# Optimization experiments

Hardware: AMD Instinct MI355X
Metric: run time of the kernel (lower is better)

The kernel has to match this reference:

```python
import jax, jax.numpy as jnp
import numpy as np

N_CLASSES = 1000  # init kwarg n_classes
BIG = 1e24        # diagonal fill used by get_center_distances


def setup_inputs() -> dict:
    key = jax.random.key(0)
    k1, k2 = jax.random.split(key)
    embeddings = jax.random.normal(k1, (400000, 64), dtype=jnp.float32)
    target = jax.random.randint(k2, (400000,), 0, N_CLASSES)
    return {"embeddings": embeddings, "target": target}


def reference(embeddings, target):
    # Training-mode IILoss forward (returned loss does not depend on running buffers).
    n = embeddings.shape[0]
    ones = jnp.ones((n,), embeddings.dtype)
    counts = jax.ops.segment_sum(ones, target, num_segments=N_CLASSES)          # [C]
    sums = jax.ops.segment_sum(embeddings, target, num_segments=N_CLASSES)      # [C, D]
    mu = sums / jnp.maximum(counts, 1.0)[:, None]                                # per-class mean

    # intra_spread = sum_i ||e_i - mu[target_i]||^2 / n  (single fused pass)
    diff = embeddings - mu[target]
    intra_spread = jnp.sum(diff * diff) / n

    # pairwise squared distances between centers of classes present in the batch
    sq = jnp.sum(mu * mu, axis=1)                                                # [C]
    dists = sq[:, None] + sq[None, :] - 2.0 * (mu @ mu.T)                        # [C, C]
    present = counts > 0
    mask = present[:, None] & present[None, :] & ~jnp.eye(N_CLASSES, dtype=bool)
    dists = jnp.where(mask, dists, jnp.asarray(BIG, dists.dtype))
    inter_separation = -jnp.min(dists)
    return (intra_spread, inter_separation)
```

## Files before the change

kernel.cpp:

```cpp
#include <hip/hip_runtime.h>

#define NCLS 1000
#define DIM 64
#define CURW 32
#define SPLIT 4

struct Ws {
    int      counts[NCLS];
    unsigned minkey;
    unsigned pad_;
    int      offs[NCLS];
    float    mu[NCLS * DIM];
    float    sq[NCLS];
    int      cur[NCLS * CURW];
};

__device__ __forceinline__ unsigned fkey(float x) {
    unsigned b = __float_as_uint(x);
    return (b & 0x80000000u) ? ~b : (b | 0x80000000u);
}
__device__ __forceinline__ float funkey(unsigned k) {
    return (k & 0x80000000u) ? __uint_as_float(k & 0x7FFFFFFFu)
                             : __uint_as_float(~k);
}

__global__ __launch_bounds__(256) void k_hist(const int* __restrict__ tgt, int n, Ws* ws) {
    __shared__ int h[NCLS];
    for (int i = threadIdx.x; i < NCLS; i += 256) h[i] = 0;
    __syncthreads();
    const int n4 = n >> 2;
    const int4* t4 = reinterpret_cast<const int4*>(tgt);
    for (int i = blockIdx.x * 256 + threadIdx.x; i < n4; i += gridDim.x * 256) {
        const int4 v = t4[i];
        atomicAdd(&h[v.x], 1); atomicAdd(&h[v.y], 1);
        atomicAdd(&h[v.z], 1); atomicAdd(&h[v.w], 1);
    }
    if (blockIdx.x == 0)
        for (int r = (n4 << 2) + threadIdx.x; r < n; r += 256) atomicAdd(&h[tgt[r]], 1);
    __syncthreads();
    for (int i = threadIdx.x; i < NCLS; i += 256) {
        const int c = h[i];
        if (c) atomicAdd(&ws->counts[i], c);
    }
}

__global__ __launch_bounds__(1024) void k_scan(Ws* ws) {
    __shared__ int s[1024];
    const int t = threadIdx.x;
    const int myc = (t < NCLS) ? ws->counts[t] : 0;
    s[t] = myc;
    __syncthreads();
    for (int st = 1; st < 1024; st <<= 1) {
        const int v = (t >= st) ? s[t - st] : 0;
        __syncthreads();
        s[t] += v;
        __syncthreads();
    }
    if (t < NCLS) {
        const int e = s[t] - myc;
        ws->offs[t] = e;
        ws->cur[t * CURW] = e;
    }
    if (t == 0) ws->minkey = fkey(1.0e24f);
}

__global__ __launch_bounds__(256) void k_scatter(const int* __restrict__ tgt, int n,
                                                 Ws* ws, int* __restrict__ idxs) {
    for (int r = blockIdx.x * 256 + threadIdx.x; r < n; r += gridDim.x * 256) {
        const int p = atomicAdd(&ws->cur[tgt[r] * CURW], 1);
        idxs[p] = r;
    }
}

__global__ __launch_bounds__(256) void k_reduce(const float* __restrict__ emb,
                                                const int* __restrict__ idxs,
                                                const Ws* __restrict__ ws,
                                                float* __restrict__ part,
                                                float* __restrict__ part_ssq) {
    __shared__ float lds[16][DIM + 4];
    __shared__ float ssq_red[4];
    const int bid  = blockIdx.x;
    const int c    = bid >> 2;
    const int sp   = bid & (SPLIT - 1);
    const int t    = threadIdx.x;
    const int slot = t & 15;
    const int g    = t >> 4;
    const int cnt  = ws->counts[c];
    const int i0   = (cnt * sp) / SPLIT;
    const int i1   = (cnt * (sp + 1)) / SPLIT;
    const int base = ws->offs[c] + i0;
    const int m    = i1 - i0;

    float ax = 0.f, ay = 0.f, az = 0.f, aw = 0.f;
    float ssq = 0.f;
    int i = g;
    for (; i + 16 < m; i += 32) {
        const int r0 = idxs[base + i];
        const int r1 = idxs[base + i + 16];
        const float4 v0 = *reinterpret_cast<const float4*>(emb + (size_t)r0 * DIM + slot * 4);
        const float4 v1 = *reinterpret_cast<const float4*>(emb + (size_t)r1 * DIM + slot * 4);
        ax += v0.x; ay += v0.y; az += v0.z; aw += v0.w;
        ax += v1.x; ay += v1.y; az += v1.z; aw += v1.w;
        ssq += v0.x * v0.x + v0.y * v0.y + v0.z * v0.z + v0.w * v0.w
             + v1.x * v1.x + v1.y * v1.y + v1.z * v1.z + v1.w * v1.w;
    }
    if (i < m) {
        const int r0 = idxs[base + i];
        const float4 v0 = *reinterpret_cast<const float4*>(emb + (size_t)r0 * DIM + slot * 4);
        ax += v0.x; ay += v0.y; az += v0.z; aw += v0.w;
        ssq += v0.x * v0.x + v0.y * v0.y + v0.z * v0.z + v0.w * v0.w;
    }
    lds[g][slot * 4 + 0] = ax; lds[g][slot * 4 + 1] = ay;
    lds[g][slot * 4 + 2] = az; lds[g][slot * 4 + 3] = aw;
    __syncthreads();
    for (int s = 8; s >= 1; s >>= 1) {
        if (g < s) {
            #pragma unroll
            for (int k = 0; k < 4; ++k)
                lds[g][slot * 4 + k] += lds[g + s][slot * 4 + k];
        }
        __syncthreads();
    }
    for (int o = 32; o; o >>= 1) ssq += __shfl_down(ssq, o);
    if ((t & 63) == 0) ssq_red[t >> 6] = ssq;
    __syncthreads();
    if (t < DIM) part[bid * DIM + t] = lds[0][t];
    if (t == 0)
        part_ssq[bid] = ssq_red[0] + ssq_red[1] + ssq_red[2] + ssq_red[3];
}

__global__ __launch_bounds__(64) void k_centers(Ws* ws,
                                                const float* __restrict__ part,
                                                const float* __restrict__ part_ssq,
                                                float* __restrict__ cls_ssq,
                                                float* __restrict__ cls_mt) {
    const int c = blockIdx.x;
    const int t = threadIdx.x;
    const int cnt = ws->counts[c];
    float v = 0.f;
    #pragma unroll
    for (int s = 0; s < SPLIT; ++s) v += part[(c * SPLIT + s) * DIM + t];
    const float m = v / (float)max(cnt, 1);
    ws->mu[c * DIM + t] = m;
    float p = m * m;
    for (int o = 32; o; o >>= 1) p += __shfl_down(p, o);
    if (t == 0) {
        ws->sq[c] = p;
        cls_mt[c] = cnt ? (float)cnt * p : 0.f;
        float s2 = 0.f;
        #pragma unroll
        for (int s = 0; s < SPLIT; ++s) s2 += part_ssq[c * SPLIT + s];
        cls_ssq[c] = s2;
    }
}

#define TILE 64
#define NTA 16
#define NPAIR (NTA * (NTA + 1) / 2)
__global__ __launch_bounds__(256) void k_pairs(Ws* ws) {
    __shared__ float As[TILE][DIM + 4];
    __shared__ float Bst[DIM][TILE + 1];
    __shared__ float sqa_s[TILE], sqb_s[TILE];
    __shared__ int   pa_s[TILE], pb_s[TILE];
    __shared__ unsigned redm[4];

    int rem = blockIdx.x, ta = 0;
    while (rem >= NTA - ta) { rem -= NTA - ta; ++ta; }
    const int tb = ta + rem;
    const int tid = threadIdx.x;

    for (int i = tid; i < TILE * (DIM / 4); i += 256) {
        const int r = i >> 4, c4 = (i & 15) * 4;
        const int ga = ta * TILE + r;
        const int gb = tb * TILE + r;
        float4 va = make_float4(0.f, 0.f, 0.f, 0.f);
        float4 vb = make_float4(0.f, 0.f, 0.f, 0.f);
        if (ga < NCLS) va = *reinterpret_cast<const float4*>(&ws->mu[ga * DIM + c4]);
        if (gb < NCLS) vb = *reinterpret_cast<const float4*>(&ws->mu[gb * DIM + c4]);
        *reinterpret_cast<float4*>(&As[r][c4]) = va;
        Bst[c4 + 0][r] = vb.x; Bst[c4 + 1][r] = vb.y;
        Bst[c4 + 2][r] = vb.z; Bst[c4 + 3][r] = vb.w;
    }
    if (tid < TILE) {
        const int ga = ta * TILE + tid;
        const int gb = tb * TILE + tid;
        pa_s[tid]  = (ga < NCLS) ? (ws->counts[ga] > 0) : 0;
        sqa_s[tid] = (ga < NCLS) ? ws->sq[ga] : 0.f;
        pb_s[tid]  = (gb < NCLS) ? (ws->counts[gb] > 0) : 0;
        sqb_s[tid] = (gb < NCLS) ? ws->sq[gb] : 0.f;
    }
    __syncthreads();

    const int ty4 = (tid >> 4) * 4;
    const int tx4 = (tid & 15) * 4;
    float dot[4][4];
    #pragma unroll
    for (int i = 0; i < 4; ++i)
        #pragma unroll
        for (int j = 0; j < 4; ++j) dot[i][j] = 0.f;

    #pragma unroll 8
    for (int k = 0; k < DIM; ++k) {
        float av[4], bv[4];
        #pragma unroll
        for (int i = 0; i < 4; ++i) av[i] = As[ty4 + i][k];
        #pragma unroll
        for (int j = 0; j < 4; ++j) bv[j] = Bst[k][tx4 + j];
        #pragma unroll
        for (int i = 0; i < 4; ++i)
            #pragma unroll
            for (int j = 0; j < 4; ++j) dot[i][j] += av[i] * bv[j];
    }

    float best = 3.0e38f;
    #pragma unroll
    for (int i = 0; i < 4; ++i) {
        #pragma unroll
        for (int j = 0; j < 4; ++j) {
            const int ga = ta * TILE + ty4 + i;
            const int gb = tb * TILE + tx4 + j;
            const bool valid = pa_s[ty4 + i] && pb_s[tx4 + j] && (ga != gb);
            const float dd = sqa_s[ty4 + i] + sqb_s[tx4 + j] - 2.f * dot[i][j];
            if (valid) best = fminf(best, dd);
        }
    }
    for (int off = 32; off; off >>= 1) best = fminf(best, __shfl_down(best, off));
    if ((tid & 63) == 0) redm[tid >> 6] = fkey(best);
    __syncthreads();
    if (tid == 0) {
        unsigned m = redm[0];
        #pragma unroll
        for (int w = 1; w < 4; ++w) m = min(m, redm[w]);
        atomicMin(&ws->minkey, m);
    }
}

__global__ __launch_bounds__(256) void k_final(const Ws* ws,
                                               const float* __restrict__ cls_ssq,
                                               const float* __restrict__ cls_mt,
                                               float* out, int n) {
    __shared__ double sd[256], md[256];
    const int t = threadIdx.x;
    double a = 0.0, b = 0.0;
    for (int i = t; i < NCLS; i += 256) { a += (double)cls_ssq[i]; b += (double)cls_mt[i]; }
    sd[t] = a; md[t] = b;
    __syncthreads();
    for (int s = 128; s >= 1; s >>= 1) {
        if (t < s) { sd[t] += sd[t + s]; md[t] += md[t + s]; }
        __syncthreads();
    }
    if (t == 0) {
        out[0] = (float)((sd[0] - md[0]) / (double)n);
        out[1] = -funkey(ws->minkey);
    }
}

extern "C" void kernel_launch(void* const* d_in, const int* in_sizes, int n_in,
                              void* d_out, int out_size, void* d_ws, size_t ws_size,
                              hipStream_t stream) {
    const float* emb = (const float*)d_in[0];
    const int*   tgt = (const int*)d_in[1];
    float* out = (float*)d_out;
    const int n = in_sizes[1];
    Ws* ws = (Ws*)d_ws;
    char* p = (char*)d_ws + sizeof(Ws);
    int*   idxs     = (int*)p;                 p += (size_t)n * sizeof(int);
    float* part     = (float*)p;               p += (size_t)NCLS * SPLIT * DIM * sizeof(float);
    float* part_ssq = (float*)p;               p += (size_t)NCLS * SPLIT * sizeof(float);
    float* cls_ssq  = (float*)p;               p += (size_t)NCLS * sizeof(float);
    float* cls_mt   = (float*)p;

    hipMemsetAsync(d_ws, 0, offsetof(Ws, minkey), stream);
    k_hist   <<<256, 256, 0, stream>>>(tgt, n, ws);
    k_scan   <<<1, 1024, 0, stream>>>(ws);
    k_scatter<<<1024, 256, 0, stream>>>(tgt, n, ws, idxs);
    k_reduce <<<NCLS * SPLIT, 256, 0, stream>>>(emb, idxs, ws, part, part_ssq);
    k_centers<<<NCLS, 64, 0, stream>>>(ws, part, part_ssq, cls_ssq, cls_mt);
    k_pairs  <<<NPAIR, 256, 0, stream>>>(ws);
    k_final  <<<1, 256, 0, stream>>>(ws, cls_ssq, cls_mt, out, n);
}
```

Baseline: 72.18 us.

## Stage class indices in LDS and gather rows per wavefront with 8-way unroll

Result: no change. 72.16 us (-0.0%).

```diff
diff --git a/kernel.cpp b/kernel.cpp
--- a/kernel.cpp
+++ b/kernel.cpp
@@ -4,6 +4,7 @@
 #define DIM 64
 #define CURW 32
 #define SPLIT 4
+#define STAGE 512
 
 struct Ws {
     int      counts[NCLS];
@@ -24,6 +25,11 @@
                              : __uint_as_float(~k);
 }
 
+__global__ __launch_bounds__(256) void k_zero(Ws* ws) {
+    const int t = blockIdx.x * 256 + threadIdx.x;
+    if (t < NCLS) ws->counts[t] = 0;
+}
+
 __global__ __launch_bounds__(256) void k_hist(const int* __restrict__ tgt, int n, Ws* ws) {
     __shared__ int h[NCLS];
     for (int i = threadIdx.x; i < NCLS; i += 256) h[i] = 0;
@@ -77,56 +83,60 @@
                                                 const Ws* __restrict__ ws,
                                                 float* __restrict__ part,
                                                 float* __restrict__ part_ssq) {
-    __shared__ float lds[16][DIM + 4];
-    __shared__ float ssq_red[4];
+    __shared__ int   sidx[STAGE];
+    __shared__ float facc[4][DIM];
+    __shared__ float fssq[4];
     const int bid  = blockIdx.x;
     const int c    = bid >> 2;
     const int sp   = bid & (SPLIT - 1);
     const int t    = threadIdx.x;
-    const int slot = t & 15;
-    const int g    = t >> 4;
+    const int lane = t & 63;
+    const int w    = t >> 6;
     const int cnt  = ws->counts[c];
     const int i0   = (cnt * sp) / SPLIT;
     const int i1   = (cnt * (sp + 1)) / SPLIT;
     const int base = ws->offs[c] + i0;
     const int m    = i1 - i0;
 
-    float ax = 0.f, ay = 0.f, az = 0.f, aw = 0.f;
-    float ssq = 0.f;
-    int i = g;
-    for (; i + 16 < m; i += 32) {
-        const int r0 = idxs[base + i];
-        const int r1 = idxs[base + i + 16];
-        const float4 v0 = *reinterpret_cast<const float4*>(emb + (size_t)r0 * DIM + slot * 4);
-        const float4 v1 = *reinterpret_cast<const float4*>(emb + (size_t)r1 * DIM + slot * 4);
-        ax += v0.x; ay += v0.y; az += v0.z; aw += v0.w;
-        ax += v1.x; ay += v1.y; az += v1.z; aw += v1.w;
-        ssq += v0.x * v0.x + v0.y * v0.y + v0.z * v0.z + v0.w * v0.w
-             + v1.x * v1.x + v1.y * v1.y + v1.z * v1.z + v1.w * v1.w;
-    }
-    if (i < m) {
-        const int r0 = idxs[base + i];
-        const float4 v0 = *reinterpret_cast<const float4*>(emb + (size_t)r0 * DIM + slot * 4);
-        ax += v0.x; ay += v0.y; az += v0.z; aw += v0.w;
-        ssq += v0.x * v0.x + v0.y * v0.y + v0.z * v0.z + v0.w * v0.w;
-    }
-    lds[g][slot * 4 + 0] = ax; lds[g][slot * 4 + 1] = ay;
-    lds[g][slot * 4 + 2] = az; lds[g][slot * 4 + 3] = aw;
-    __syncthreads();
-    for (int s = 8; s >= 1; s >>= 1) {
-        if (g < s) {
-            #pragma unroll
-            for (int k = 0; k < 4; ++k)
-                lds[g][slot * 4 + k] += lds[g + s][slot * 4 + k];
+    float acc = 0.f, ssq = 0.f;
+    for (int s0 = 0; s0 < m; s0 += STAGE) {
+        const int mm = min(STAGE, m - s0);
+        __syncthreads();
+        for (int i = t; i < mm; i += 256) sidx[i] = idxs[base + s0 + i];
+        __syncthreads();
+        int p = w;
+        for (; p + 28 < mm; p += 32) {
+            const int r0 = sidx[p];      const int r1 = sidx[p + 4];
+            const int r2 = sidx[p + 8];  const int r3 = sidx[p + 12];
+            const int r4 = sidx[p + 16]; const int r5 = sidx[p + 20];
+            const int r6 = sidx[p + 24]; const int r7 = sidx[p + 28];
+            const float v0 = emb[(size_t)r0 * DIM + lane];
+            const float v1 = emb[(size_t)r1 * DIM + lane];
+            const float v2 = emb[(size_t)r2 * DIM + lane];
+            const float v3 = emb[(size_t)r3 * DIM + lane];
+            const float v4 = emb[(size_t)r4 * DIM + lane];
+            const float v5 = emb[(size_t)r5 * DIM + lane];
+            const float v6 = emb[(size_t)r6 * DIM + lane];
+            const float v7 = emb[(size_t)r7 * DIM + lane];
+            acc += v0 + v1 + v2 + v3 + v4 + v5 + v6 + v7;
+            ssq += v0 * v0 + v1 * v1 + v2 * v2 + v3 * v3
+                 + v4 * v4 + v5 * v5 + v6 * v6 + v7 * v7;
         }
-        __syncthreads();
-    }
+        for (; p < mm; p += 4) {
+            const int r0 = sidx[p];
+            const float v0 = emb[(size_t)r0 * DIM + lane];
+            acc += v0;
+            ssq += v0 * v0;
+        }
+    }
+    facc[w][lane] = acc;
     for (int o = 32; o; o >>= 1) ssq += __shfl_down(ssq, o);
-    if ((t & 63) == 0) ssq_red[t >> 6] = ssq;
-    __syncthreads();
-    if (t < DIM) part[bid * DIM + t] = lds[0][t];
+    if (lane == 0) fssq[w] = ssq;
+    __syncthreads();
+    if (t < DIM)
+        part[bid * DIM + t] = facc[0][t] + facc[1][t] + facc[2][t] + facc[3][t];
     if (t == 0)
-        part_ssq[bid] = ssq_red[0] + ssq_red[1] + ssq_red[2] + ssq_red[3];
+        part_ssq[bid] = fssq[0] + fssq[1] + fssq[2] + fssq[3];
 }
 
 __global__ __launch_bounds__(64) void k_centers(Ws* ws,
@@ -270,7 +280,7 @@
     float* cls_ssq  = (float*)p;               p += (size_t)NCLS * sizeof(float);
     float* cls_mt   = (float*)p;
 
-    hipMemsetAsync(d_ws, 0, offsetof(Ws, minkey), stream);
+    k_zero   <<<4, 256, 0, stream>>>(ws);
     k_hist   <<<256, 256, 0, stream>>>(tgt, n, ws);
     k_scan   <<<1, 1024, 0, stream>>>(ws);
     k_scatter<<<1024, 256, 0, stream>>>(tgt, n, ws, idxs);
```
